# Performance work log

Hardware: AMD Instinct MI355X
Metric: run time of the kernel (lower is better)

## Reference

```python
import jax, jax.numpy as jnp
import numpy as np

NUM_LAYERS = 4
INPUT_DIM = 512
BATCH = 16384


def setup_inputs() -> dict:
    key = jax.random.key(0)
    kx, kw, kb = jax.random.split(key, 3)
    x = jax.random.normal(kx, (BATCH, INPUT_DIM), dtype=jnp.float32)
    # PyTorch nn.Linear init: U(-1/sqrt(fan_in), 1/sqrt(fan_in))
    bound = 1.0 / np.sqrt(INPUT_DIM)
    W = jax.random.uniform(kw, (NUM_LAYERS, INPUT_DIM, INPUT_DIM), jnp.float32, -bound, bound)
    b = jax.random.uniform(kb, (NUM_LAYERS, INPUT_DIM), jnp.float32, -bound, bound)
    return {"x": x, "W": W, "b": b}


def reference(x, W, b):
    # x: [B, D]; W: [L, D, D] (torch Linear weight, so y = x @ W_i.T + b_i)
    x_list = [x]
    for i in range(NUM_LAYERS):
        x_ = x_list[-1]
        # sequentially accumulate dot-product residuals against all prior activations
        for x_pre in x_list[:-1]:
            s = jnp.sum(x_ * x_pre, axis=-1, keepdims=True)  # [B, 1]
            x_ = x_ + s
        y = jnp.einsum("bd,ed->be", x_, W[i]) + b[i]  # Linear: x_ @ W_i.T + b_i
        x_list.append(y)
    out = jnp.concatenate(x_list[1:], axis=-1)  # [B, L*D]
    return out
```

## Files before the change

### kernel.cpp

```cpp
#include <hip/hip_runtime.h>
#include <stdint.h>


#define BROWS 16384
#define DIM 512
#define NL 4
#define OUTSTRIDE (NL * DIM)

#define BM 128
#define BN 128
#define BK 32

typedef unsigned short ushort_t;
typedef __attribute__((ext_vector_type(8))) short bf16x8;
typedef __attribute__((ext_vector_type(4))) float f32x4;

__device__ inline ushort_t f32_to_bf16(float f) {
    union { float f; uint32_t u; } v; v.f = f;
    uint32_t u = v.u;
    uint32_t r = (u + 0x7fffu + ((u >> 16) & 1u)) >> 16;
    return (ushort_t)r;
}

__device__ inline float bf16_bits_to_f32(ushort_t u) {
    union { uint32_t u; float f; } v; v.u = ((uint32_t)u) << 16; return v.f;
}

__device__ inline float wave_reduce_sum(float v) {
    #pragma unroll
    for (int off = 32; off > 0; off >>= 1) v += __shfl_down(v, off, 64);
    return v;
}

__global__ __launch_bounds__(256) void convw_kernel(
    const float* __restrict__ W, ushort_t* __restrict__ Wb,
    float* __restrict__ wsum)
{
    int row = blockIdx.x;
    int t = threadIdx.x;
    const float* wp = W + (size_t)row * DIM;
    float f0 = wp[2 * t], f1 = wp[2 * t + 1];
    ushort_t* wbp = Wb + (size_t)row * DIM;
    wbp[2 * t]     = f32_to_bf16(f0);
    wbp[2 * t + 1] = f32_to_bf16(f1);
    __shared__ float red[4];
    int wave = t >> 6, lane = t & 63;
    float r = wave_reduce_sum(f0 + f1);
    if (lane == 0) red[wave] = r;
    __syncthreads();
    if (t == 0) wsum[row] = red[0] + red[1] + red[2] + red[3];
}

__global__ __launch_bounds__(256) void conv0_kernel(
    const float* __restrict__ x0, ushort_t* __restrict__ xb0,
    float* __restrict__ sums)
{
    int wave = threadIdx.x >> 6, lane = threadIdx.x & 63;
    int b = blockIdx.x * 4 + wave;
    const float* xp = x0 + (size_t)b * DIM + lane * 8;
    float4 a = ((const float4*)xp)[0];
    float4 c4 = ((const float4*)xp)[1];
    float f[8] = {a.x, a.y, a.z, a.w, c4.x, c4.y, c4.z, c4.w};
    bf16x8 o;
    float s = 0.f;
    #pragma unroll
    for (int i = 0; i < 8; ++i) {
        o[i] = (short)f32_to_bf16(f[i]);
        s += f[i];
    }
    *(bf16x8*)(xb0 + (size_t)b * DIM + lane * 8) = o;
    s = wave_reduce_sum(s);
    if (lane == 0) sums[b] = s;
}

__global__ __launch_bounds__(256) void dots_kernel(
    const ushort_t* __restrict__ xb, float* __restrict__ sums,
    float* __restrict__ cvals, int lp1)
{
    int wave = threadIdx.x >> 6, lane = threadIdx.x & 63;
    int b = blockIdx.x * 4 + wave;
    bf16x8 v = *(const bf16x8*)(xb + ((size_t)lp1 * BROWS + b) * DIM + lane * 8);
    float xi[8];
    float ssum = 0.f;
    #pragma unroll
    for (int i = 0; i < 8; ++i) {
        xi[i] = bf16_bits_to_f32((ushort_t)v[i]);
        ssum += xi[i];
    }
    float dots[3] = {0.f, 0.f, 0.f};
    #pragma unroll
    for (int j = 0; j < 3; ++j) {
        if (j < lp1) {
            bf16x8 w = *(const bf16x8*)(xb + ((size_t)j * BROWS + b) * DIM + lane * 8);
            float d = 0.f;
            #pragma unroll
            for (int i = 0; i < 8; ++i)
                d += xi[i] * bf16_bits_to_f32((ushort_t)w[i]);
            dots[j] = d;
        }
    }
    ssum = wave_reduce_sum(ssum);
    #pragma unroll
    for (int j = 0; j < 3; ++j)
        dots[j] = wave_reduce_sum(dots[j]);
    if (lane == 0) {
        sums[lp1 * BROWS + b] = ssum;
        float c = 0.f;
        for (int j = 0; j < lp1; ++j)
            c = c + dots[j] + c * sums[j * BROWS + b];
        cvals[lp1 * BROWS + b] = c;
    }
}

__global__ __launch_bounds__(256) void gemm_kernel(
    const ushort_t* __restrict__ A,
    const ushort_t* __restrict__ Wb,
    const float* __restrict__ bias,
    const float* __restrict__ wsum,
    const float* __restrict__ cvals,
    float* __restrict__ out,
    ushort_t* __restrict__ xb_next)
{
    __shared__ __align__(16) ushort_t sA[BM * BK];
    __shared__ __align__(16) ushort_t sB[BN * BK];

    int tid  = threadIdx.x;
    int wave = tid >> 6;
    int lane = tid & 63;
    int wm = wave >> 1, wn = wave & 1;
    int bm = blockIdx.y * BM;
    int bn = blockIdx.x * BN;

    f32x4 acc[4][4] = {};

    int srow = lane >> 2;
    int scol = (lane & 3) * 8;

    for (int k0 = 0; k0 < DIM; k0 += BK) {
        __syncthreads();
        #pragma unroll
        for (int t2 = 0; t2 < 2; ++t2) {
            int r = wave * 32 + t2 * 16;
            const ushort_t* gA = A  + (size_t)(bm + r + srow) * DIM + k0 + scol;
            const ushort_t* gB = Wb + (size_t)(bn + r + srow) * DIM + k0 + scol;
            __builtin_amdgcn_global_load_lds(
                (const __attribute__((address_space(1))) void*)gA,
                (__attribute__((address_space(3))) void*)(sA + r * BK), 16, 0, 0);
            __builtin_amdgcn_global_load_lds(
                (const __attribute__((address_space(1))) void*)gB,
                (__attribute__((address_space(3))) void*)(sB + r * BK), 16, 0, 0);
        }
        __syncthreads();

        int q = lane >> 4;
        int rr = lane & 15;
        bf16x8 af[4], bfr[4];
        #pragma unroll
        for (int mi = 0; mi < 4; ++mi)
            af[mi] = *(const bf16x8*)(sA + (wm * 64 + mi * 16 + rr) * BK + q * 8);
        #pragma unroll
        for (int ni = 0; ni < 4; ++ni)
            bfr[ni] = *(const bf16x8*)(sB + (wn * 64 + ni * 16 + rr) * BK + q * 8);
        #pragma unroll
        for (int mi = 0; mi < 4; ++mi)
            #pragma unroll
            for (int ni = 0; ni < 4; ++ni)
                acc[mi][ni] = __builtin_amdgcn_mfma_f32_16x16x32_bf16(
                    af[mi], bfr[ni], acc[mi][ni], 0, 0, 0);
    }

    int q = lane >> 4, nlane = lane & 15;
    #pragma unroll
    for (int ni = 0; ni < 4; ++ni) {
        int n_g = bn + wn * 64 + ni * 16 + nlane;
        float ws = wsum[n_g];
        float bs = bias[n_g];
        #pragma unroll
        for (int mi = 0; mi < 4; ++mi) {
            int m_base = bm + wm * 64 + mi * 16 + q * 4;
            #pragma unroll
            for (int r = 0; r < 4; ++r) {
                int m_g = m_base + r;
                float c = cvals ? cvals[m_g] : 0.f;
                float v = acc[mi][ni][r] + c * ws + bs;
                out[(size_t)m_g * OUTSTRIDE + n_g] = v;
                if (xb_next)
                    xb_next[(size_t)m_g * DIM + n_g] = f32_to_bf16(v);
            }
        }
    }
}

extern "C" void kernel_launch(void* const* d_in, const int* in_sizes, int n_in,
                              void* d_out, int out_size, void* d_ws, size_t ws_size,
                              hipStream_t stream) {
    (void)in_sizes; (void)n_in; (void)out_size; (void)ws_size;
    const float* x0   = (const float*)d_in[0];
    const float* W    = (const float*)d_in[1];
    const float* bias = (const float*)d_in[2];
    float* out = (float*)d_out;

    char* ws = (char*)d_ws;
    ushort_t* xb   = (ushort_t*)ws;
    ushort_t* Wb   = (ushort_t*)(ws + 67108864);
    float*    wsum = (float*)   (ws + 69206016);
    float*    sums = (float*)   (ws + 69214208);
    float*    cvals= (float*)   (ws + 69476352);

    convw_kernel<<<NL * DIM, 256, 0, stream>>>(W, Wb, wsum);
    conv0_kernel<<<BROWS / 4, 256, 0, stream>>>(x0, xb, sums);

    dim3 ggrid(DIM / BN, BROWS / BM);
    for (int l = 0; l < NL; ++l) {
        gemm_kernel<<<ggrid, 256, 0, stream>>>(
            xb + (size_t)l * BROWS * DIM,
            Wb + (size_t)l * DIM * DIM,
            bias + l * DIM,
            wsum + l * DIM,
            (l > 0) ? (cvals + l * BROWS) : nullptr,
            out + l * DIM,
            (l < NL - 1) ? (xb + (size_t)(l + 1) * BROWS * DIM) : nullptr);
        if (l < NL - 1)
            dots_kernel<<<BROWS / 4, 256, 0, stream>>>(xb, sums, cvals, l + 1);
    }
}
```

Baseline: 291.8 us.

## Fuse dot-product residual computation into GEMM epilogue and merge prep kernels

Removes the separate dots kernel. Each GEMM epilogue now computes partial row sums and dot products of its fp32 output tile against earlier bf16 activations, then accumulates them with atomics into workspace buffers. The next layer's GEMM rebuilds the per-row correction scalar from these buffers at block start. The two conversion kernels are merged into one prep kernel, which also zeroes the atomic targets. This cuts launches and avoids rereading activations in a separate pass, at the cost of uncoalesced scalar bf16 loads in the epilogue, atomics, and slightly different rounding, since dots now use fp32 outputs instead of bf16.

```diff
diff --git a/kernel.cpp b/kernel.cpp
--- a/kernel.cpp
+++ b/kernel.cpp
@@ -32,32 +32,39 @@
     return v;
 }
 
-__global__ __launch_bounds__(256) void convw_kernel(
-    const float* __restrict__ W, ushort_t* __restrict__ Wb,
-    float* __restrict__ wsum)
+__device__ inline float quad16_reduce(float v) {
+    #pragma unroll
+    for (int off = 8; off > 0; off >>= 1) v += __shfl_xor(v, off, 64);
+    return v;
+}
+
+__global__ __launch_bounds__(256) void prep_kernel(
+    const float* __restrict__ x0, const float* __restrict__ W,
+    ushort_t* __restrict__ xb0, ushort_t* __restrict__ Wb,
+    float* __restrict__ wsum, float* __restrict__ sums,
+    float* __restrict__ zbase)
 {
-    int row = blockIdx.x;
-    int t = threadIdx.x;
-    const float* wp = W + (size_t)row * DIM;
-    float f0 = wp[2 * t], f1 = wp[2 * t + 1];
-    ushort_t* wbp = Wb + (size_t)row * DIM;
-    wbp[2 * t]     = f32_to_bf16(f0);
-    wbp[2 * t + 1] = f32_to_bf16(f1);
-    __shared__ float red[4];
-    int wave = t >> 6, lane = t & 63;
-    float r = wave_reduce_sum(f0 + f1);
-    if (lane == 0) red[wave] = r;
-    __syncthreads();
-    if (t == 0) wsum[row] = red[0] + red[1] + red[2] + red[3];
-}
-
-__global__ __launch_bounds__(256) void conv0_kernel(
-    const float* __restrict__ x0, ushort_t* __restrict__ xb0,
-    float* __restrict__ sums)
-{
+    int blk = blockIdx.x;
     int wave = threadIdx.x >> 6, lane = threadIdx.x & 63;
-    int b = blockIdx.x * 4 + wave;
-    const float* xp = x0 + (size_t)b * DIM + lane * 8;
+    if (blk >= 4608) {
+        int idx = (blk - 4608) * 1024 + threadIdx.x * 4;
+        float4 z = {0.f, 0.f, 0.f, 0.f};
+        *(float4*)(zbase + idx) = z;
+        return;
+    }
+    const float* src; ushort_t* dst; float* red_out; int row;
+    if (blk < 4096) {
+        row = blk * 4 + wave;
+        src = x0 + (size_t)row * DIM;
+        dst = xb0 + (size_t)row * DIM;
+        red_out = sums;
+    } else {
+        row = (blk - 4096) * 4 + wave;
+        src = W + (size_t)row * DIM;
+        dst = Wb + (size_t)row * DIM;
+        red_out = wsum;
+    }
+    const float* xp = src + lane * 8;
     float4 a = ((const float4*)xp)[0];
     float4 c4 = ((const float4*)xp)[1];
     float f[8] = {a.x, a.y, a.z, a.w, c4.x, c4.y, c4.z, c4.w};
@@ -68,61 +75,27 @@
         o[i] = (short)f32_to_bf16(f[i]);
         s += f[i];
     }
-    *(bf16x8*)(xb0 + (size_t)b * DIM + lane * 8) = o;
+    *(bf16x8*)(dst + lane * 8) = o;
     s = wave_reduce_sum(s);
-    if (lane == 0) sums[b] = s;
-}
-
-__global__ __launch_bounds__(256) void dots_kernel(
-    const ushort_t* __restrict__ xb, float* __restrict__ sums,
-    float* __restrict__ cvals, int lp1)
-{
-    int wave = threadIdx.x >> 6, lane = threadIdx.x & 63;
-    int b = blockIdx.x * 4 + wave;
-    bf16x8 v = *(const bf16x8*)(xb + ((size_t)lp1 * BROWS + b) * DIM + lane * 8);
-    float xi[8];
-    float ssum = 0.f;
-    #pragma unroll
-    for (int i = 0; i < 8; ++i) {
-        xi[i] = bf16_bits_to_f32((ushort_t)v[i]);
-        ssum += xi[i];
-    }
-    float dots[3] = {0.f, 0.f, 0.f};
-    #pragma unroll
-    for (int j = 0; j < 3; ++j) {
-        if (j < lp1) {
-            bf16x8 w = *(const bf16x8*)(xb + ((size_t)j * BROWS + b) * DIM + lane * 8);
-            float d = 0.f;
-            #pragma unroll
-            for (int i = 0; i < 8; ++i)
-                d += xi[i] * bf16_bits_to_f32((ushort_t)w[i]);
-            dots[j] = d;
-        }
-    }
-    ssum = wave_reduce_sum(ssum);
-    #pragma unroll
-    for (int j = 0; j < 3; ++j)
-        dots[j] = wave_reduce_sum(dots[j]);
-    if (lane == 0) {
-        sums[lp1 * BROWS + b] = ssum;
-        float c = 0.f;
-        for (int j = 0; j < lp1; ++j)
-            c = c + dots[j] + c * sums[j * BROWS + b];
-        cvals[lp1 * BROWS + b] = c;
-    }
+    if (lane == 0) red_out[row] = s;
 }
 
 __global__ __launch_bounds__(256) void gemm_kernel(
-    const ushort_t* __restrict__ A,
+    const ushort_t* __restrict__ xb,
     const ushort_t* __restrict__ Wb,
     const float* __restrict__ bias,
     const float* __restrict__ wsum,
-    const float* __restrict__ cvals,
+    float* __restrict__ sums,
+    float* __restrict__ dots,
     float* __restrict__ out,
-    ushort_t* __restrict__ xb_next)
+    ushort_t* __restrict__ xb_next,
+    int l)
 {
     __shared__ __align__(16) ushort_t sA[BM * BK];
     __shared__ __align__(16) ushort_t sB[BN * BK];
+    __shared__ float cv[BM];
+    __shared__ float redS[2][BM];
+    __shared__ float redD[2][BM][3];
 
     int tid  = threadIdx.x;
     int wave = tid >> 6;
@@ -130,9 +103,19 @@
     int wm = wave >> 1, wn = wave & 1;
     int bm = blockIdx.y * BM;
     int bn = blockIdx.x * BN;
+    const ushort_t* A = xb + (size_t)l * BROWS * DIM;
+
+    if (tid < BM) {
+        float c = 0.f;
+        if (l > 0) {
+            const float* db = dots + (size_t)(l - 1) * 3 * BROWS;
+            for (int j = 0; j < l; ++j)
+                c = c + db[j * BROWS + bm + tid] + c * sums[j * BROWS + bm + tid];
+        }
+        cv[tid] = c;
+    }
 
     f32x4 acc[4][4] = {};
-
     int srow = lane >> 2;
     int scol = (lane & 3) * 8;
 
@@ -177,16 +160,61 @@
         float bs = bias[n_g];
         #pragma unroll
         for (int mi = 0; mi < 4; ++mi) {
-            int m_base = bm + wm * 64 + mi * 16 + q * 4;
             #pragma unroll
             for (int r = 0; r < 4; ++r) {
-                int m_g = m_base + r;
-                float c = cvals ? cvals[m_g] : 0.f;
-                float v = acc[mi][ni][r] + c * ws + bs;
-                out[(size_t)m_g * OUTSTRIDE + n_g] = v;
+                int m_l = wm * 64 + mi * 16 + q * 4 + r;
+                float v = acc[mi][ni][r] + cv[m_l] * ws + bs;
+                acc[mi][ni][r] = v;
+                out[(size_t)(bm + m_l) * OUTSTRIDE + n_g] = v;
                 if (xb_next)
-                    xb_next[(size_t)m_g * DIM + n_g] = f32_to_bf16(v);
+                    xb_next[(size_t)(bm + m_l) * DIM + n_g] = f32_to_bf16(v);
             }
+        }
+    }
+
+    if (l < 3) {
+        bool need_sums = (l <= 1);
+        if (need_sums) {
+            #pragma unroll
+            for (int mi = 0; mi < 4; ++mi) {
+                #pragma unroll
+                for (int r = 0; r < 4; ++r) {
+                    float p = acc[mi][0][r] + acc[mi][1][r] + acc[mi][2][r] + acc[mi][3][r];
+                    p = quad16_reduce(p);
+                    if (nlane == 0)
+                        redS[wn][wm * 64 + mi * 16 + q * 4 + r] = p;
+                }
+            }
+        }
+        for (int j = 0; j <= l; ++j) {
+            const ushort_t* xj = xb + (size_t)j * BROWS * DIM;
+            #pragma unroll
+            for (int mi = 0; mi < 4; ++mi) {
+                #pragma unroll
+                for (int r = 0; r < 4; ++r) {
+                    int m_l = wm * 64 + mi * 16 + q * 4 + r;
+                    const ushort_t* xr = xj + (size_t)(bm + m_l) * DIM;
+                    float pd = 0.f;
+                    #pragma unroll
+                    for (int ni = 0; ni < 4; ++ni) {
+                        int n_g = bn + wn * 64 + ni * 16 + nlane;
+                        pd += acc[mi][ni][r] * bf16_bits_to_f32(xr[n_g]);
+                    }
+                    pd = quad16_reduce(pd);
+                    if (nlane == 0)
+                        redD[wn][m_l][j] = pd;
+                }
+            }
+        }
+        __syncthreads();
+        if (tid < BM) {
+            int m_g = bm + tid;
+            if (need_sums)
+                atomicAdd(&sums[(size_t)(l + 1) * BROWS + m_g],
+                          redS[0][tid] + redS[1][tid]);
+            for (int j = 0; j <= l; ++j)
+                atomicAdd(&dots[((size_t)l * 3 + j) * BROWS + m_g],
+                          redD[0][tid][j] + redD[1][tid][j]);
         }
     }
 }
@@ -205,22 +233,21 @@
     ushort_t* Wb   = (ushort_t*)(ws + 67108864);
     float*    wsum = (float*)   (ws + 69206016);
     float*    sums = (float*)   (ws + 69214208);
-    float*    cvals= (float*)   (ws + 69476352);
-
-    convw_kernel<<<NL * DIM, 256, 0, stream>>>(W, Wb, wsum);
-    conv0_kernel<<<BROWS / 4, 256, 0, stream>>>(x0, xb, sums);
+    float*    dots = (float*)   (ws + 69476352);
+
+    prep_kernel<<<4800, 256, 0, stream>>>(x0, W, xb, Wb, wsum, sums,
+                                          sums + BROWS);
 
     dim3 ggrid(DIM / BN, BROWS / BM);
     for (int l = 0; l < NL; ++l) {
         gemm_kernel<<<ggrid, 256, 0, stream>>>(
-            xb + (size_t)l * BROWS * DIM,
+            xb,
             Wb + (size_t)l * DIM * DIM,
             bias + l * DIM,
             wsum + l * DIM,
-            (l > 0) ? (cvals + l * BROWS) : nullptr,
+            sums, dots,
             out + l * DIM,
-            (l < NL - 1) ? (xb + (size_t)(l + 1) * BROWS * DIM) : nullptr);
-        if (l < NL - 1)
-            dots_kernel<<<BROWS / 4, 256, 0, stream>>>(xb, sums, cvals, l + 1);
-    }
-}
+            (l < NL - 1) ? (xb + (size_t)(l + 1) * BROWS * DIM) : nullptr,
+            l);
+    }
+}
```

New measurement: 298.6 us. 1.02x slower.
